# Kernel optimization log

Measured on AMD Instinct MI355X. Metric: run time of the kernel, lower is better.

Reference implementation:

```python
import jax, jax.numpy as jnp
import numpy as np

DIM_SPATIAL = 4096
DIM_QK = 256
DIM_V = 256
BATCH = 8
HW = 64  # sqrt(DIM_SPATIAL)


def setup_inputs() -> dict:
    key = jax.random.key(0)
    k1, k2, k3, k4, k5 = jax.random.split(key, 5)
    return {
        "queries": jax.random.normal(k1, (BATCH, DIM_QK, HW, HW), dtype=jnp.float32),
        "keys": jax.random.normal(k2, (BATCH, DIM_QK, HW, HW), dtype=jnp.float32),
        "values": jax.random.normal(k3, (BATCH, DIM_V, HW, HW), dtype=jnp.float32),
        "q_pos_embedding": jax.random.normal(k4, (1, DIM_SPATIAL, DIM_QK), dtype=jnp.float32) * 0.05,
        "k_pos_embedding": jax.random.normal(k5, (1, DIM_SPATIAL, DIM_QK), dtype=jnp.float32) * 0.05,
    }


def reference(queries, keys, values, q_pos_embedding, k_pos_embedding):
    scale = jnp.sqrt(jnp.float32(DIM_QK))
    # [B, C, H, W] -> [B, N, C] with N = H*W
    q = queries.reshape(-1, DIM_QK, DIM_SPATIAL).transpose(0, 2, 1) + q_pos_embedding
    k = keys.reshape(-1, DIM_QK, DIM_SPATIAL).transpose(0, 2, 1) + k_pos_embedding
    v = values.reshape(-1, DIM_V, DIM_SPATIAL).transpose(0, 2, 1)
    # [B, N, N] attention
    dots = jnp.einsum("bqc,bkc->bqk", q, k) / scale
    attn = jax.nn.softmax(dots, axis=-1)
    out = jnp.einsum("bqk,bkc->bqc", attn, v)  # [B, N, Cv]
    out = out.transpose(0, 2, 1).reshape(-1, DIM_V, HW, HW)
    return out
```

## Files before the change

kernel.cpp:

```cpp
#include <hip/hip_runtime.h>
#include <hip/hip_bf16.h>

typedef short short8 __attribute__((ext_vector_type(8)));
typedef float f32x16 __attribute__((ext_vector_type(16)));
typedef unsigned int u32x4 __attribute__((ext_vector_type(4)));

#define NB 8
#define NN 4096
#define NC 256
#define KBLK 64
#define NT (NN / KBLK)

#define V_OFF 32768
#define BUF_BYTES 65536
#define ML_OFF 131072
#define SMEM_BYTES (ML_OFF + 1024)

typedef __attribute__((address_space(3))) unsigned char lds_uc;
typedef __attribute__((address_space(1))) const unsigned char glb_uc;

__device__ __forceinline__ void gload_lds16(const void* g, void* l) {
    __builtin_amdgcn_global_load_lds((const glb_uc*)g, (lds_uc*)l, 16, 0, 0);
}

__device__ __forceinline__ unsigned short f2bf(float f) {
    unsigned int u = __float_as_uint(f);
    u += 0x7fffu + ((u >> 16) & 1u);
    return (unsigned short)(u >> 16);
}

__global__ void tp_kernel(const float* __restrict__ src, const float* __restrict__ pos,
                          unsigned short* __restrict__ dst, float scale) {
    __shared__ float tile[64][65];
    const int n0 = blockIdx.x * 64;
    const int c0 = blockIdx.y * 64;
    const int b  = blockIdx.z;
    const int nl = threadIdx.x & 63;
    const int cq = threadIdx.x >> 6;
    #pragma unroll
    for (int i = 0; i < 16; ++i) {
        int cc = cq + i * 4;
        tile[cc][nl] = src[((size_t)(b * NC + c0 + cc)) * NN + n0 + nl];
    }
    __syncthreads();
    #pragma unroll
    for (int i = 0; i < 16; ++i) {
        int nn = cq + i * 4;
        float v = tile[nl][nn] + pos[(size_t)(n0 + nn) * NC + c0 + nl];
        dst[((size_t)(b * NN + n0 + nn)) * NC + c0 + nl] = f2bf(v * scale);
    }
}

__global__ void castv_kernel(const float4* __restrict__ src, ushort4* __restrict__ dst, int n4) {
    int i = blockIdx.x * 256 + threadIdx.x;
    if (i >= n4) return;
    float4 v = src[i];
    ushort4 o;
    o.x = f2bf(v.x); o.y = f2bf(v.y); o.z = f2bf(v.z); o.w = f2bf(v.w);
    dst[i] = o;
}

__global__ __launch_bounds__(512, 1) void attn_kernel(const unsigned short* __restrict__ qb,
                                                      const unsigned short* __restrict__ kb,
                                                      const unsigned short* __restrict__ vt,
                                                      float* __restrict__ out) {
    __shared__ __align__(16) unsigned char smem[SMEM_BYTES];
    const int tid  = threadIdx.x;
    const int w    = tid >> 6;
    const int lane = tid & 63;
    const int q5   = lane & 31;
    const int hi2  = lane >> 5;
    const int qg   = w >> 1;
    const int kh   = w & 1;
    const int qt   = blockIdx.x >> 3;
    const int b    = blockIdx.x & 7;

    short8 qf[16];
    {
        const unsigned short* qr = qb + ((size_t)(b * NN + qt * 128 + qg * 32 + q5)) * NC + hi2 * 8;
        #pragma unroll
        for (int kk = 0; kk < 16; ++kk) qf[kk] = *(const short8*)(qr + kk * 16);
    }

    const char* kbb = (const char*)(kb + (size_t)b * NN * NC);
    const char* vbb = (const char*)(vt + (size_t)b * NC * NN);
    unsigned kof[4];
    {
        unsigned x16 = (unsigned)(q5 * 16);
        #pragma unroll
        for (int j = 0; j < 4; ++j) {
            unsigned row = (unsigned)(w * 8 + j * 2 + hi2);
            kof[j] = row * 512 + (x16 ^ ((row & 7) << 4));
        }
    }
    unsigned vof;
    {
        unsigned r3 = (unsigned)(lane >> 3);
        vof = (unsigned)(w * 32 + r3) * 8192 + (((unsigned)((lane & 7) * 16)) ^ ((r3 & 7) << 4));
    }

    unsigned ka[4], va0, va1;
    {
        unsigned krow = (unsigned)(kh * 32 + q5);
        unsigned ksw  = (krow & 7) << 4;
        #pragma unroll
        for (int j = 0; j < 4; ++j)
            ka[j] = krow * 512 + (((unsigned)(j * 32 + hi2 * 16)) ^ ksw);
        unsigned vsw = ((unsigned)q5 & 7) << 4;
        va0 = V_OFF + (unsigned)q5 * 128 + (((unsigned)(kh * 64 + 0  + hi2 * 16)) ^ vsw);
        va1 = V_OFF + (unsigned)q5 * 128 + (((unsigned)(kh * 64 + 32 + hi2 * 16)) ^ vsw);
    }

    f32x16 acc[8];
    #pragma unroll
    for (int t = 0; t < 8; ++t)
        #pragma unroll
        for (int r = 0; r < 16; ++r) acc[t][r] = 0.f;
    float lsum = 0.f;

    {
        #pragma unroll
        for (int i = 0; i < 4; ++i) {
            gload_lds16(kbb + kof[i],                            smem + (w * 4 + i) * 1024);
            gload_lds16(vbb + vof + (size_t)i * 65536,           smem + V_OFF + (w * 4 + i) * 1024);
        }
    }
    __syncthreads();

    for (int kt = 0; kt < NT; ++kt) {
        const unsigned bb = (unsigned)(kt & 1) * BUF_BYTES;
        if (kt + 1 < NT) {
            const unsigned nb = bb ^ BUF_BYTES;
            const char* kp = kbb + (size_t)(kt + 1) * (KBLK * NC * 2);
            const char* vp = vbb + vof + (size_t)(kt + 1) * (KBLK * 2);
            #pragma unroll
            for (int i = 0; i < 4; ++i) {
                gload_lds16(kp + kof[i],                  smem + nb + (w * 4 + i) * 1024);
                gload_lds16(vp + (size_t)i * 65536,       smem + nb + V_OFF + (w * 4 + i) * 1024);
            }
        }

        f32x16 s;
        #pragma unroll
        for (int r = 0; r < 16; ++r) s[r] = 0.f;
        #pragma unroll
        for (int kk = 0; kk < 16; ++kk) {
            short8 kf = *(const short8*)(smem + bb + ka[kk & 3] + (kk >> 2) * 128);
            s = __builtin_amdgcn_mfma_f32_32x32x16_bf16(kf, qf[kk], s, 0, 0, 0);
        }

        float ps = 0.f;
        #pragma unroll
        for (int i = 0; i < 16; ++i) { s[i] = exp2f(s[i]); ps += s[i]; }
        ps += __shfl_xor(ps, 32);
        lsum += ps;

        unsigned c0, c1, c2, c3, c4, c5, c6, c7;
        asm("v_cvt_pk_bf16_f32 %0, %1, %2" : "=v"(c0) : "v"(s[0]),  "v"(s[1]));
        asm("v_cvt_pk_bf16_f32 %0, %1, %2" : "=v"(c1) : "v"(s[2]),  "v"(s[3]));
        asm("v_cvt_pk_bf16_f32 %0, %1, %2" : "=v"(c2) : "v"(s[4]),  "v"(s[5]));
        asm("v_cvt_pk_bf16_f32 %0, %1, %2" : "=v"(c3) : "v"(s[6]),  "v"(s[7]));
        asm("v_cvt_pk_bf16_f32 %0, %1, %2" : "=v"(c4) : "v"(s[8]),  "v"(s[9]));
        asm("v_cvt_pk_bf16_f32 %0, %1, %2" : "=v"(c5) : "v"(s[10]), "v"(s[11]));
        asm("v_cvt_pk_bf16_f32 %0, %1, %2" : "=v"(c6) : "v"(s[12]), "v"(s[13]));
        asm("v_cvt_pk_bf16_f32 %0, %1, %2" : "=v"(c7) : "v"(s[14]), "v"(s[15]));
        asm("v_permlane32_swap_b32 %0, %1" : "+v"(c0), "+v"(c2));
        asm("v_permlane32_swap_b32 %0, %1" : "+v"(c1), "+v"(c3));
        asm("v_permlane32_swap_b32 %0, %1" : "+v"(c4), "+v"(c6));
        asm("v_permlane32_swap_b32 %0, %1" : "+v"(c5), "+v"(c7));
        u32x4 w0 = {c0, c1, c2, c3};
        u32x4 w1 = {c4, c5, c6, c7};
        short8 pf0 = __builtin_bit_cast(short8, w0);
        short8 pf1 = __builtin_bit_cast(short8, w1);

        #pragma unroll
        for (int t = 0; t < 8; ++t) {
            short8 vf0 = *(const short8*)(smem + bb + va0 + t * 4096);
            acc[t] = __builtin_amdgcn_mfma_f32_32x32x16_bf16(vf0, pf0, acc[t], 0, 0, 0);
            short8 vf1 = *(const short8*)(smem + bb + va1 + t * 4096);
            acc[t] = __builtin_amdgcn_mfma_f32_32x32x16_bf16(vf1, pf1, acc[t], 0, 0, 0);
        }

        __syncthreads();
    }

    {
        float* ml = (float*)(smem + ML_OFF);
        ml[(qg * 2 + kh) * 32 + q5] = lsum;
    }
    __syncthreads();
    float lp = ((const float*)(smem + ML_OFF))[(qg * 2 + (kh ^ 1)) * 32 + q5];
    float L  = lsum + lp;

    if (kh == 1) {
        #pragma unroll
        for (int t = 0; t < 8; ++t)
            #pragma unroll
            for (int r = 0; r < 16; ++r) {
                int dvl = (r & 3) + 8 * (r >> 2) + hi2 * 4;
                *(float*)(smem + qg * 32768 + t * 4096 + dvl * 128 + q5 * 4) = acc[t][r];
            }
    }
    __syncthreads();
    if (kh == 0) {
        float invL = 1.0f / L;
        const size_t obase = (size_t)b * NC * NN + (size_t)(qt * 128 + qg * 32) + q5;
        #pragma unroll
        for (int t = 0; t < 8; ++t)
            #pragma unroll
            for (int r = 0; r < 16; ++r) {
                int dvl = (r & 3) + 8 * (r >> 2) + hi2 * 4;
                float po = *(const float*)(smem + qg * 32768 + t * 4096 + dvl * 128 + q5 * 4);
                float val = (acc[t][r] + po) * invL;
                out[obase + (size_t)(t * 32 + dvl) * NN] = val;
            }
    }
}

extern "C" void kernel_launch(void* const* d_in, const int* in_sizes, int n_in,
                              void* d_out, int out_size, void* d_ws, size_t ws_size,
                              hipStream_t stream) {
    (void)in_sizes; (void)n_in; (void)out_size; (void)ws_size;
    const float* q    = (const float*)d_in[0];
    const float* k    = (const float*)d_in[1];
    const float* v    = (const float*)d_in[2];
    const float* qpos = (const float*)d_in[3];
    const float* kpos = (const float*)d_in[4];

    unsigned short* qb = (unsigned short*)d_ws;
    unsigned short* kb = qb + (size_t)NB * NN * NC;
    unsigned short* vt = kb + (size_t)NB * NN * NC;

    const float qscale = 0.09016844005556021f;

    tp_kernel<<<dim3(64, 4, NB), 256, 0, stream>>>(q, qpos, qb, qscale);
    tp_kernel<<<dim3(64, 4, NB), 256, 0, stream>>>(k, kpos, kb, 1.0f);
    castv_kernel<<<dim3((NB * NC * NN / 4) / 256), 256, 0, stream>>>((const float4*)v, (ushort4*)vt, NB * NC * NN / 4);
    attn_kernel<<<dim3(256), 512, 0, stream>>>(qb, kb, vt, (float*)d_out);
}
```

Baseline: 175.7 us.

## Pre-tile V into MFMA fragment order and load it directly into registers

A new preprocessing kernel converts V to bf16 already laid out in per-lane MFMA fragment order for each 64-key block. The attention kernel then reads V fragments straight from global memory into registers instead of staging them through LDS, which halves LDS use and allows launch bounds of two blocks per CU. The q and k transpose launches are merged into one grid, and the epilogue is split into two passes so it fits in the smaller LDS. The trade-offs are extra register pressure from 16 V fragments per iteration and global-load latency on the critical path of the PV MFMAs, while the grid is still only 256 blocks.

New measurement: 274.4 us. 1.56x slower.

```diff
diff --git a/kernel.cpp b/kernel.cpp
--- a/kernel.cpp
+++ b/kernel.cpp
@@ -11,9 +11,8 @@
 #define KBLK 64
 #define NT (NN / KBLK)
 
-#define V_OFF 32768
-#define BUF_BYTES 65536
-#define ML_OFF 131072
+#define BUF_BYTES 32768
+#define ML_OFF 65536
 #define SMEM_BYTES (ML_OFF + 1024)
 
 typedef __attribute__((address_space(3))) unsigned char lds_uc;
@@ -29,12 +28,20 @@
     return (unsigned short)(u >> 16);
 }
 
-__global__ void tp_kernel(const float* __restrict__ src, const float* __restrict__ pos,
-                          unsigned short* __restrict__ dst, float scale) {
+__global__ void tp_kernel(const float* __restrict__ qsrc, const float* __restrict__ ksrc,
+                          const float* __restrict__ qpos, const float* __restrict__ kpos,
+                          unsigned short* __restrict__ qdst, unsigned short* __restrict__ kdst,
+                          float qscale) {
     __shared__ float tile[64][65];
+    const int z = blockIdx.z;
+    const int b = z & 7;
+    const bool isq = z < 8;
+    const float* src = isq ? qsrc : ksrc;
+    const float* pos = isq ? qpos : kpos;
+    unsigned short* dst = isq ? qdst : kdst;
+    const float scale = isq ? qscale : 1.0f;
     const int n0 = blockIdx.x * 64;
     const int c0 = blockIdx.y * 64;
-    const int b  = blockIdx.z;
     const int nl = threadIdx.x & 63;
     const int cq = threadIdx.x >> 6;
     #pragma unroll
@@ -51,18 +58,35 @@
     }
 }
 
-__global__ void castv_kernel(const float4* __restrict__ src, ushort4* __restrict__ dst, int n4) {
-    int i = blockIdx.x * 256 + threadIdx.x;
-    if (i >= n4) return;
-    float4 v = src[i];
-    ushort4 o;
-    o.x = f2bf(v.x); o.y = f2bf(v.y); o.z = f2bf(v.z); o.w = f2bf(v.w);
-    dst[i] = o;
-}
-
-__global__ __launch_bounds__(512, 1) void attn_kernel(const unsigned short* __restrict__ qb,
+__global__ void vtile_kernel(const float* __restrict__ src, unsigned short* __restrict__ dst) {
+    __shared__ float lds[256][66];
+    const int kt  = blockIdx.x;
+    const int b   = blockIdx.y;
+    const int tid = threadIdx.x;
+    #pragma unroll 4
+    for (int rep = 0; rep < 64; ++rep) {
+        int c = rep * 4 + (tid >> 6);
+        int key = tid & 63;
+        lds[c][key] = src[((size_t)(b * NC + c)) * NN + kt * KBLK + key];
+    }
+    __syncthreads();
+    const int w = tid >> 6, l = tid & 63;
+    #pragma unroll
+    for (int rr = 0; rr < 8; ++rr) {
+        int rec = w * 8 + rr;
+        int kh = rec >> 4, t = (rec >> 1) & 7, ks = rec & 1;
+        int ch = t * 32 + (l & 31);
+        int k0 = kh * 32 + ks * 16 + (l >> 5) * 8;
+        short8 o;
+        #pragma unroll
+        for (int j = 0; j < 8; ++j) o[j] = (short)f2bf(lds[ch][k0 + j]);
+        *(short8*)(dst + ((((size_t)b * NT + kt) * 32 + rec) * 64 + l) * 8) = o;
+    }
+}
+
+__global__ __launch_bounds__(512, 2) void attn_kernel(const unsigned short* __restrict__ qb,
                                                       const unsigned short* __restrict__ kb,
-                                                      const unsigned short* __restrict__ vt,
+                                                      const unsigned short* __restrict__ vt2,
                                                       float* __restrict__ out) {
     __shared__ __align__(16) unsigned char smem[SMEM_BYTES];
     const int tid  = threadIdx.x;
@@ -83,7 +107,7 @@
     }
 
     const char* kbb = (const char*)(kb + (size_t)b * NN * NC);
-    const char* vbb = (const char*)(vt + (size_t)b * NC * NN);
+    const char* vtb = (const char*)vt2 + (size_t)b * NT * 32768;
     unsigned kof[4];
     {
         unsigned x16 = (unsigned)(q5 * 16);
@@ -93,22 +117,14 @@
             kof[j] = row * 512 + (x16 ^ ((row & 7) << 4));
         }
     }
-    unsigned vof;
-    {
-        unsigned r3 = (unsigned)(lane >> 3);
-        vof = (unsigned)(w * 32 + r3) * 8192 + (((unsigned)((lane & 7) * 16)) ^ ((r3 & 7) << 4));
-    }
-
-    unsigned ka[4], va0, va1;
+
+    unsigned ka[4];
     {
         unsigned krow = (unsigned)(kh * 32 + q5);
         unsigned ksw  = (krow & 7) << 4;
         #pragma unroll
         for (int j = 0; j < 4; ++j)
             ka[j] = krow * 512 + (((unsigned)(j * 32 + hi2 * 16)) ^ ksw);
-        unsigned vsw = ((unsigned)q5 & 7) << 4;
-        va0 = V_OFF + (unsigned)q5 * 128 + (((unsigned)(kh * 64 + 0  + hi2 * 16)) ^ vsw);
-        va1 = V_OFF + (unsigned)q5 * 128 + (((unsigned)(kh * 64 + 32 + hi2 * 16)) ^ vsw);
     }
 
     f32x16 acc[8];
@@ -118,13 +134,9 @@
         for (int r = 0; r < 16; ++r) acc[t][r] = 0.f;
     float lsum = 0.f;
 
-    {
-        #pragma unroll
-        for (int i = 0; i < 4; ++i) {
-            gload_lds16(kbb + kof[i],                            smem + (w * 4 + i) * 1024);
-            gload_lds16(vbb + vof + (size_t)i * 65536,           smem + V_OFF + (w * 4 + i) * 1024);
-        }
-    }
+    #pragma unroll
+    for (int i = 0; i < 4; ++i)
+        gload_lds16(kbb + kof[i], smem + (w * 4 + i) * 1024);
     __syncthreads();
 
     for (int kt = 0; kt < NT; ++kt) {
@@ -132,13 +144,16 @@
         if (kt + 1 < NT) {
             const unsigned nb = bb ^ BUF_BYTES;
             const char* kp = kbb + (size_t)(kt + 1) * (KBLK * NC * 2);
-            const char* vp = vbb + vof + (size_t)(kt + 1) * (KBLK * 2);
             #pragma unroll
-            for (int i = 0; i < 4; ++i) {
-                gload_lds16(kp + kof[i],                  smem + nb + (w * 4 + i) * 1024);
-                gload_lds16(vp + (size_t)i * 65536,       smem + nb + V_OFF + (w * 4 + i) * 1024);
-            }
-        }
+            for (int i = 0; i < 4; ++i)
+                gload_lds16(kp + kof[i], smem + nb + (w * 4 + i) * 1024);
+        }
+
+        const char* vr = vtb + (size_t)kt * 32768 + (unsigned)(kh * 16384 + lane * 16);
+        short8 vfr[16];
+        #pragma unroll
+        for (int r2 = 0; r2 < 16; ++r2)
+            vfr[r2] = *(const short8*)(vr + r2 * 1024);
 
         f32x16 s;
         #pragma unroll
@@ -175,10 +190,8 @@
 
         #pragma unroll
         for (int t = 0; t < 8; ++t) {
-            short8 vf0 = *(const short8*)(smem + bb + va0 + t * 4096);
-            acc[t] = __builtin_amdgcn_mfma_f32_32x32x16_bf16(vf0, pf0, acc[t], 0, 0, 0);
-            short8 vf1 = *(const short8*)(smem + bb + va1 + t * 4096);
-            acc[t] = __builtin_amdgcn_mfma_f32_32x32x16_bf16(vf1, pf1, acc[t], 0, 0, 0);
+            acc[t] = __builtin_amdgcn_mfma_f32_32x32x16_bf16(vfr[2 * t],     pf0, acc[t], 0, 0, 0);
+            acc[t] = __builtin_amdgcn_mfma_f32_32x32x16_bf16(vfr[2 * t + 1], pf1, acc[t], 0, 0, 0);
         }
 
         __syncthreads();
@@ -190,30 +203,33 @@
     }
     __syncthreads();
     float lp = ((const float*)(smem + ML_OFF))[(qg * 2 + (kh ^ 1)) * 32 + q5];
-    float L  = lsum + lp;
-
-    if (kh == 1) {
-        #pragma unroll
-        for (int t = 0; t < 8; ++t)
+    float L    = lsum + lp;
+    float invL = 1.0f / L;
+    const size_t obase = (size_t)b * NC * NN + (size_t)(qt * 128 + qg * 32) + q5;
+
+    #pragma unroll
+    for (int p = 0; p < 2; ++p) {
+        __syncthreads();
+        if (kh == 1 && (qg >> 1) == p) {
             #pragma unroll
-            for (int r = 0; r < 16; ++r) {
-                int dvl = (r & 3) + 8 * (r >> 2) + hi2 * 4;
-                *(float*)(smem + qg * 32768 + t * 4096 + dvl * 128 + q5 * 4) = acc[t][r];
-            }
-    }
-    __syncthreads();
-    if (kh == 0) {
-        float invL = 1.0f / L;
-        const size_t obase = (size_t)b * NC * NN + (size_t)(qt * 128 + qg * 32) + q5;
-        #pragma unroll
-        for (int t = 0; t < 8; ++t)
+            for (int t = 0; t < 8; ++t)
+                #pragma unroll
+                for (int r = 0; r < 16; ++r) {
+                    int dvl = (r & 3) + 8 * (r >> 2) + hi2 * 4;
+                    *(float*)(smem + (qg & 1) * 32768 + t * 4096 + dvl * 128 + q5 * 4) = acc[t][r];
+                }
+        }
+        __syncthreads();
+        if (kh == 0 && (qg >> 1) == p) {
             #pragma unroll
-            for (int r = 0; r < 16; ++r) {
-                int dvl = (r & 3) + 8 * (r >> 2) + hi2 * 4;
-                float po = *(const float*)(smem + qg * 32768 + t * 4096 + dvl * 128 + q5 * 4);
-                float val = (acc[t][r] + po) * invL;
-                out[obase + (size_t)(t * 32 + dvl) * NN] = val;
-            }
+            for (int t = 0; t < 8; ++t)
+                #pragma unroll
+                for (int r = 0; r < 16; ++r) {
+                    int dvl = (r & 3) + 8 * (r >> 2) + hi2 * 4;
+                    float po = *(const float*)(smem + (qg & 1) * 32768 + t * 4096 + dvl * 128 + q5 * 4);
+                    out[obase + (size_t)(t * 32 + dvl) * NN] = (acc[t][r] + po) * invL;
+                }
+        }
     }
 }
 
@@ -227,14 +243,13 @@
     const float* qpos = (const float*)d_in[3];
     const float* kpos = (const float*)d_in[4];
 
-    unsigned short* qb = (unsigned short*)d_ws;
-    unsigned short* kb = qb + (size_t)NB * NN * NC;
-    unsigned short* vt = kb + (size_t)NB * NN * NC;
+    unsigned short* qb  = (unsigned short*)d_ws;
+    unsigned short* kb  = qb + (size_t)NB * NN * NC;
+    unsigned short* vt2 = kb + (size_t)NB * NN * NC;
 
     const float qscale = 0.09016844005556021f;
 
-    tp_kernel<<<dim3(64, 4, NB), 256, 0, stream>>>(q, qpos, qb, qscale);
-    tp_kernel<<<dim3(64, 4, NB), 256, 0, stream>>>(k, kpos, kb, 1.0f);
-    castv_kernel<<<dim3((NB * NC * NN / 4) / 256), 256, 0, stream>>>((const float4*)v, (ushort4*)vt, NB * NC * NN / 4);
-    attn_kernel<<<dim3(256), 512, 0, stream>>>(qb, kb, vt, (float*)d_out);
-}
+    tp_kernel<<<dim3(64, 4, 16), 256, 0, stream>>>(q, k, qpos, kpos, qb, kb, qscale);
+    vtile_kernel<<<dim3(NT, NB), 256, 0, stream>>>(v, vt2);
+    attn_kernel<<<dim3(256), 512, 0, stream>>>(qb, kb, vt2, (float*)d_out);
+}
```

## Widen LDS swizzles for K/V tiles, merge Q/K transpose launches, split epilogue

Applied to the files above, without the earlier changes.

Replaces the 8-way XOR swizzle on the K and V LDS tiles with a 32-way swizzle and recomputes the matching global-load offsets and fragment read addresses. The goal is fewer LDS bank conflicts in the MFMA operand reads. It also fuses the Q and K transpose/cast kernels into a single launch with a doubled grid z dimension. The epilogue reduction is split into two phases that reuse a smaller LDS region, which adds extra barriers.

Measured after the change: 185.6 us. 1.06x slower.

```diff
diff --git a/kernel.cpp b/kernel.cpp
--- a/kernel.cpp
+++ b/kernel.cpp
@@ -29,12 +29,20 @@
     return (unsigned short)(u >> 16);
 }
 
-__global__ void tp_kernel(const float* __restrict__ src, const float* __restrict__ pos,
-                          unsigned short* __restrict__ dst, float scale) {
+__global__ void tp_kernel(const float* __restrict__ qsrc, const float* __restrict__ ksrc,
+                          const float* __restrict__ qpos, const float* __restrict__ kpos,
+                          unsigned short* __restrict__ qdst, unsigned short* __restrict__ kdst,
+                          float qscale) {
     __shared__ float tile[64][65];
+    const int z = blockIdx.z;
+    const int b = z & 7;
+    const bool isq = z < 8;
+    const float* src = isq ? qsrc : ksrc;
+    const float* pos = isq ? qpos : kpos;
+    unsigned short* dst = isq ? qdst : kdst;
+    const float scale = isq ? qscale : 1.0f;
     const int n0 = blockIdx.x * 64;
     const int c0 = blockIdx.y * 64;
-    const int b  = blockIdx.z;
     const int nl = threadIdx.x & 63;
     const int cq = threadIdx.x >> 6;
     #pragma unroll
@@ -84,32 +92,22 @@
 
     const char* kbb = (const char*)(kb + (size_t)b * NN * NC);
     const char* vbb = (const char*)(vt + (size_t)b * NC * NN);
-    unsigned kof[4];
+    unsigned kof[4], vof[4];
     {
-        unsigned x16 = (unsigned)(q5 * 16);
         #pragma unroll
         for (int j = 0; j < 4; ++j) {
             unsigned row = (unsigned)(w * 8 + j * 2 + hi2);
-            kof[j] = row * 512 + (x16 ^ ((row & 7) << 4));
-        }
-    }
-    unsigned vof;
-    {
-        unsigned r3 = (unsigned)(lane >> 3);
-        vof = (unsigned)(w * 32 + r3) * 8192 + (((unsigned)((lane & 7) * 16)) ^ ((r3 & 7) << 4));
-    }
-
-    unsigned ka[4], va0, va1;
-    {
-        unsigned krow = (unsigned)(kh * 32 + q5);
-        unsigned ksw  = (krow & 7) << 4;
-        #pragma unroll
-        for (int j = 0; j < 4; ++j)
-            ka[j] = krow * 512 + (((unsigned)(j * 32 + hi2 * 16)) ^ ksw);
-        unsigned vsw = ((unsigned)q5 & 7) << 4;
-        va0 = V_OFF + (unsigned)q5 * 128 + (((unsigned)(kh * 64 + 0  + hi2 * 16)) ^ vsw);
-        va1 = V_OFF + (unsigned)q5 * 128 + (((unsigned)(kh * 64 + 32 + hi2 * 16)) ^ vsw);
-    }
+            kof[j] = row * 512 + ((((unsigned)q5) ^ (row & 31)) << 4);
+            unsigned vrow = (unsigned)((w * 4 + j) * 2 + hi2);
+            unsigned gs = ((unsigned)q5) ^ (vrow & 31);
+            vof[j] = (4 * vrow + (gs >> 3)) * 8192 + (gs & 7) * 16;
+        }
+    }
+
+    const unsigned kbase = (unsigned)(kh * 32 + q5) * 512;
+    const unsigned hq    = (unsigned)((q5 ^ hi2) << 4);
+    const unsigned vb    = (unsigned)(q5 >> 2) * 512;
+    const unsigned vx    = (unsigned)(((((q5 & 3) * 8) + kh * 4 + hi2) ^ (q5 >> 2)) << 4);
 
     f32x16 acc[8];
     #pragma unroll
@@ -118,12 +116,10 @@
         for (int r = 0; r < 16; ++r) acc[t][r] = 0.f;
     float lsum = 0.f;
 
-    {
-        #pragma unroll
-        for (int i = 0; i < 4; ++i) {
-            gload_lds16(kbb + kof[i],                            smem + (w * 4 + i) * 1024);
-            gload_lds16(vbb + vof + (size_t)i * 65536,           smem + V_OFF + (w * 4 + i) * 1024);
-        }
+    #pragma unroll
+    for (int i = 0; i < 4; ++i) {
+        gload_lds16(kbb + kof[i], smem + (w * 4 + i) * 1024);
+        gload_lds16(vbb + vof[i], smem + V_OFF + (w * 4 + i) * 1024);
     }
     __syncthreads();
 
@@ -132,11 +128,11 @@
         if (kt + 1 < NT) {
             const unsigned nb = bb ^ BUF_BYTES;
             const char* kp = kbb + (size_t)(kt + 1) * (KBLK * NC * 2);
-            const char* vp = vbb + vof + (size_t)(kt + 1) * (KBLK * 2);
+            const char* vp = vbb + (size_t)(kt + 1) * (KBLK * 2);
             #pragma unroll
             for (int i = 0; i < 4; ++i) {
-                gload_lds16(kp + kof[i],                  smem + nb + (w * 4 + i) * 1024);
-                gload_lds16(vp + (size_t)i * 65536,       smem + nb + V_OFF + (w * 4 + i) * 1024);
+                gload_lds16(kp + kof[i], smem + nb + (w * 4 + i) * 1024);
+                gload_lds16(vp + vof[i], smem + nb + V_OFF + (w * 4 + i) * 1024);
             }
         }
 
@@ -145,7 +141,7 @@
         for (int r = 0; r < 16; ++r) s[r] = 0.f;
         #pragma unroll
         for (int kk = 0; kk < 16; ++kk) {
-            short8 kf = *(const short8*)(smem + bb + ka[kk & 3] + (kk >> 2) * 128);
+            short8 kf = *(const short8*)(smem + bb + kbase + (((unsigned)(kk * 32)) ^ hq));
             s = __builtin_amdgcn_mfma_f32_32x32x16_bf16(kf, qf[kk], s, 0, 0, 0);
         }
 
@@ -175,9 +171,10 @@
 
         #pragma unroll
         for (int t = 0; t < 8; ++t) {
-            short8 vf0 = *(const short8*)(smem + bb + va0 + t * 4096);
+            const unsigned ct = ((unsigned)((t & 3) << 3)) << 4;
+            short8 vf0 = *(const short8*)(smem + bb + V_OFF + t * 4096 + vb + (vx ^ ct));
             acc[t] = __builtin_amdgcn_mfma_f32_32x32x16_bf16(vf0, pf0, acc[t], 0, 0, 0);
-            short8 vf1 = *(const short8*)(smem + bb + va1 + t * 4096);
+            short8 vf1 = *(const short8*)(smem + bb + V_OFF + t * 4096 + vb + (vx ^ ct ^ 32u));
             acc[t] = __builtin_amdgcn_mfma_f32_32x32x16_bf16(vf1, pf1, acc[t], 0, 0, 0);
         }
 
@@ -190,30 +187,33 @@
     }
     __syncthreads();
     float lp = ((const float*)(smem + ML_OFF))[(qg * 2 + (kh ^ 1)) * 32 + q5];
-    float L  = lsum + lp;
-
-    if (kh == 1) {
-        #pragma unroll
-        for (int t = 0; t < 8; ++t)
+    float L    = lsum + lp;
+    float invL = 1.0f / L;
+    const size_t obase = (size_t)b * NC * NN + (size_t)(qt * 128 + qg * 32) + q5;
+
+    #pragma unroll
+    for (int p = 0; p < 2; ++p) {
+        __syncthreads();
+        if (kh == 1 && (qg >> 1) == p) {
             #pragma unroll
-            for (int r = 0; r < 16; ++r) {
-                int dvl = (r & 3) + 8 * (r >> 2) + hi2 * 4;
-                *(float*)(smem + qg * 32768 + t * 4096 + dvl * 128 + q5 * 4) = acc[t][r];
-            }
-    }
-    __syncthreads();
-    if (kh == 0) {
-        float invL = 1.0f / L;
-        const size_t obase = (size_t)b * NC * NN + (size_t)(qt * 128 + qg * 32) + q5;
-        #pragma unroll
-        for (int t = 0; t < 8; ++t)
+            for (int t = 0; t < 8; ++t)
+                #pragma unroll
+                for (int r = 0; r < 16; ++r) {
+                    int dvl = (r & 3) + 8 * (r >> 2) + hi2 * 4;
+                    *(float*)(smem + (qg & 1) * 32768 + t * 4096 + dvl * 128 + q5 * 4) = acc[t][r];
+                }
+        }
+        __syncthreads();
+        if (kh == 0 && (qg >> 1) == p) {
             #pragma unroll
-            for (int r = 0; r < 16; ++r) {
-                int dvl = (r & 3) + 8 * (r >> 2) + hi2 * 4;
-                float po = *(const float*)(smem + qg * 32768 + t * 4096 + dvl * 128 + q5 * 4);
-                float val = (acc[t][r] + po) * invL;
-                out[obase + (size_t)(t * 32 + dvl) * NN] = val;
-            }
+            for (int t = 0; t < 8; ++t)
+                #pragma unroll
+                for (int r = 0; r < 16; ++r) {
+                    int dvl = (r & 3) + 8 * (r >> 2) + hi2 * 4;
+                    float po = *(const float*)(smem + (qg & 1) * 32768 + t * 4096 + dvl * 128 + q5 * 4);
+                    out[obase + (size_t)(t * 32 + dvl) * NN] = (acc[t][r] + po) * invL;
+                }
+        }
     }
 }
 
@@ -233,8 +233,7 @@
 
     const float qscale = 0.09016844005556021f;
 
-    tp_kernel<<<dim3(64, 4, NB), 256, 0, stream>>>(q, qpos, qb, qscale);
-    tp_kernel<<<dim3(64, 4, NB), 256, 0, stream>>>(k, kpos, kb, 1.0f);
+    tp_kernel<<<dim3(64, 4, 16), 256, 0, stream>>>(q, k, qpos, kpos, qb, kb, qscale);
     castv_kernel<<<dim3((NB * NC * NN / 4) / 256), 256, 0, stream>>>((const float4*)v, (ushort4*)vt, NB * NC * NN / 4);
     attn_kernel<<<dim3(256), 512, 0, stream>>>(qb, kb, vt, (float*)d_out);
 }
```
